# Optimization experiments

Hardware: AMD Instinct MI355X
Metric: run time of the kernel (lower is better)

Reference implementation:

```python
import jax, jax.numpy as jnp
import numpy as np

N = 5000
NFEAT = 512
NHID = 64
NHEADS = 8
NCLASS = 40
ALPHA = 0.2  # leaky relu slope
NEG_INF = -9e15


def setup_inputs() -> dict:
    key = jax.random.key(0)
    ks = jax.random.split(key, 12)
    x = jax.random.normal(ks[0], (N, NFEAT), dtype=jnp.float32)
    # binary adjacency, ~32 avg degree, with self loops
    adj = (jax.random.uniform(ks[1], (N, N)) < (32.0 / N)).astype(jnp.float32)
    adj = jnp.maximum(adj, jnp.eye(N, dtype=jnp.float32))
    s = 1.0 / np.sqrt(NFEAT)
    W_h = jax.random.uniform(ks[2], (NHEADS, NFEAT, NHID), minval=-s, maxval=s, dtype=jnp.float32)
    a_h = jax.random.uniform(ks[3], (NHEADS, 2 * NHID), minval=-s, maxval=s, dtype=jnp.float32)
    s2 = 1.0 / np.sqrt(NHID * NHEADS)
    W_o = jax.random.uniform(ks[4], (NHID * NHEADS, NHID), minval=-s2, maxval=s2, dtype=jnp.float32)
    a_o = jax.random.uniform(ks[5], (2 * NHID,), minval=-s2, maxval=s2, dtype=jnp.float32)
    s3 = 1.0 / np.sqrt(NHID)
    fc1_w = jax.random.uniform(ks[6], (NHID, 200), minval=-s3, maxval=s3, dtype=jnp.float32)
    fc1_b = jax.random.uniform(ks[7], (200,), minval=-s3, maxval=s3, dtype=jnp.float32)
    s4 = 1.0 / np.sqrt(200)
    fc2_w = jax.random.uniform(ks[8], (200, NCLASS), minval=-s4, maxval=s4, dtype=jnp.float32)
    fc2_b = jax.random.uniform(ks[9], (NCLASS,), minval=-s4, maxval=s4, dtype=jnp.float32)
    return {"x": x, "adj": adj, "W_h": W_h, "a_h": a_h, "W_o": W_o, "a_o": a_o,
            "fc1_w": fc1_w, "fc1_b": fc1_b, "fc2_w": fc2_w, "fc2_b": fc2_b}


def _masked_attention(e, adj):
    # e: [..., N, N]; mask where adj == 0, then row softmax
    e = jnp.where(adj > 0, e, NEG_INF)
    return jax.nn.softmax(e, axis=-1)


def reference(x, adj, W_h, a_h, W_o, a_o, fc1_w, fc1_b, fc2_w, fc2_b):
    # ---- multi-head GAT layer (concat=True), eval mode (dropout off) ----
    Wh = jnp.einsum('nf,hfo->hno', x, W_h)                 # [H, N, nhid]
    f1 = jnp.einsum('hno,ho->hn', Wh, a_h[:, :NHID])       # [H, N]
    f2 = jnp.einsum('hno,ho->hn', Wh, a_h[:, NHID:])       # [H, N]
    e = jax.nn.leaky_relu(f1[:, :, None] + f2[:, None, :], ALPHA)  # [H, N, N]
    att = _masked_attention(e, adj[None, :, :])
    h = jnp.einsum('hnm,hmo->hno', att, Wh)                # [H, N, nhid]
    h1 = jax.nn.elu(h).transpose(1, 0, 2).reshape(N, NHEADS * NHID)  # concat heads

    # ---- output GAT layer (concat=False) ----
    Wh2 = h1 @ W_o                                         # [N, nhid]
    g1 = Wh2 @ a_o[:NHID]                                  # [N]
    g2 = Wh2 @ a_o[NHID:]                                  # [N]
    e2 = jax.nn.leaky_relu(g1[:, None] + g2[None, :], ALPHA)
    att2 = _masked_attention(e2, adj)
    h2 = att2 @ Wh2                                        # [N, nhid]

    # ---- MLP head ----
    h3 = jax.nn.elu(h2 @ fc1_w + fc1_b)
    return h3 @ fc2_w + fc2_b                              # [N, nclass]
```

## Files before the change

kernel.cpp:

```cpp
#include <hip/hip_runtime.h>

typedef unsigned short u16;
typedef unsigned int u32;
typedef unsigned long long u64;
typedef __bf16 bf16_t;
typedef __bf16 bf16x8 __attribute__((ext_vector_type(8)));
typedef float f32x4 __attribute__((ext_vector_type(4)));
typedef u32 u32x4 __attribute__((ext_vector_type(4)));

#define NN 5000
#define NF 512
#define NH 64
#define HEADS 8
#define NCLS 40
#define CAP 128
#define LRELU 0.2f

#define CVT_BIG 320
#define CVT_GRID (CVT_BIG + 8)

__device__ __forceinline__ bool adj_is_bf16(const void* adj) {
    return ((*(const u32*)adj) & 0xFFFFu) != 0u;
}
__device__ __forceinline__ u16 rne_bf16(float f) {
    u32 u = __float_as_uint(f);
    u += 0x7FFFu + ((u >> 16) & 1u);
    return (u16)(u >> 16);
}
__device__ __forceinline__ float up_bf16(u16 h) {
    return __uint_as_float((u32)h << 16);
}
__device__ __forceinline__ u32x4 ntload4(const void* p, int idx) {
    return __builtin_nontemporal_load(((const u32x4*)p) + idx);
}

__global__ __launch_bounds__(256) void cvt(const void* __restrict__ x, const void* __restrict__ W_h,
                                           const void* __restrict__ adj,
                                           const void* a_h, const void* W_o, const void* a_o,
                                           const void* f1w, const void* f1b,
                                           const void* f2w, const void* f2b,
                                           u16* __restrict__ xc, u16* __restrict__ whc,
                                           float* a_hc, float* W_oc, float* a_oc,
                                           float* f1wc, float* f1bc, float* f2wc, float* f2bc) {
    const bool isb = adj_is_bf16(adj);
    const int b = blockIdx.x;
    if (b < CVT_BIG) {
        const int X4 = NN * NF / 4;
        const int T4 = X4 + HEADS * NF * NH / 4;
        for (int i = b * 256 + threadIdx.x; i < T4; i += CVT_BIG * 256) {
            const void* src; u16* dst; int off;
            if (i < X4) { src = x; dst = xc; off = i; }
            else        { src = W_h; dst = whc; off = i - X4; }
            ushort4 o;
            if (isb) {
                o = ((const ushort4*)src)[off];
            } else {
                u32x4 vv = ntload4(src, off);
                o.x = rne_bf16(__uint_as_float(vv[0])); o.y = rne_bf16(__uint_as_float(vv[1]));
                o.z = rne_bf16(__uint_as_float(vv[2])); o.w = rne_bf16(__uint_as_float(vv[3]));
            }
            ((ushort4*)dst)[off] = o;
        }
    } else {
        const int s0 = HEADS * 2 * NH, s1 = HEADS * NH * NH, s2 = 2 * NH,
                  s3 = NH * 200, s4 = 200, s5 = 200 * NCLS, s6 = NCLS;
        const int total = s0 + s1 + s2 + s3 + s4 + s5 + s6;
        for (int i = (b - CVT_BIG) * 256 + threadIdx.x; i < total; i += 8 * 256) {
            const void* src; float* dst; int off = i;
            if (off < s0) { src = a_h; dst = a_hc; }
            else if ((off -= s0) < s1) { src = W_o;  dst = W_oc; }
            else if ((off -= s1) < s2) { src = a_o;  dst = a_oc; }
            else if ((off -= s2) < s3) { src = f1w;  dst = f1wc; }
            else if ((off -= s3) < s4) { src = f1b;  dst = f1bc; }
            else if ((off -= s4) < s5) { src = f2w;  dst = f2wc; }
            else { off -= s5;           src = f2b;  dst = f2bc; }
            dst[off] = isb ? up_bf16(((const u16*)src)[off]) : ((const float*)src)[off];
        }
    }
}

__global__ __launch_bounds__(256) void gemm1_f(const bf16_t* __restrict__ x,
                                               const bf16_t* __restrict__ W_h,
                                               const float* __restrict__ a_h,
                                               float* __restrict__ Wh,
                                               float* __restrict__ f1,
                                               float* __restrict__ f2) {
    const int lane = threadIdx.x & 63;
    const int wid  = threadIdx.x >> 6;
    const int rg = blockIdx.x;
    const int h  = blockIdx.y;
    const int quad = lane >> 4;
    const int lr   = lane & 15;
    const int kq   = quad * 8;
    const int nCol = wid * 16 + lr;
    const bf16_t* Bh = W_h + (size_t)h * NF * NH;
    __shared__ float f1s[4][64], f2s[4][64];

    bf16x8 bfrag[16];
    #pragma unroll
    for (int s = 0; s < 16; ++s) {
        bf16x8 bb;
        #pragma unroll
        for (int j = 0; j < 8; ++j) bb[j] = Bh[(s * 32 + kq + j) * NH + nCol];
        bfrag[s] = bb;
    }
    const float a1c = a_h[h * 128 + nCol];
    const float a2c = a_h[h * 128 + NH + nCol];

    for (int t = 0; t < 4; ++t) {
        const int rb = rg * 64 + t * 16;
        int row  = rb + lr;
        int rowc = row < NN ? row : NN - 1;
        const bf16_t* xp = x + (size_t)rowc * NF + kq;
        f32x4 acc = {0.f, 0.f, 0.f, 0.f};
        #pragma unroll
        for (int s = 0; s < 16; ++s) {
            bf16x8 a = *(const bf16x8*)(xp + s * 32);
            acc = __builtin_amdgcn_mfma_f32_16x16x32_bf16(a, bfrag[s], acc, 0, 0, 0);
        }
        #pragma unroll
        for (int r = 0; r < 4; ++r) {
            int gr = rb + quad * 4 + r;
            if (gr < NN) Wh[(size_t)gr * (HEADS * NH) + h * NH + nCol] = acc[r];
            float p1 = acc[r] * a1c, p2 = acc[r] * a2c;
            #pragma unroll
            for (int o = 8; o; o >>= 1) { p1 += __shfl_xor(p1, o); p2 += __shfl_xor(p2, o); }
            if (lr == 0) { f1s[wid][t * 16 + quad * 4 + r] = p1; f2s[wid][t * 16 + quad * 4 + r] = p2; }
        }
    }
    __syncthreads();
    if (wid == 0) {
        int gr = rg * 64 + lane;
        if (gr < NN) {
            f1[h * NN + gr] = f1s[0][lane] + f1s[1][lane] + f1s[2][lane] + f1s[3][lane];
            f2[h * NN + gr] = f2s[0][lane] + f2s[1][lane] + f2s[2][lane] + f2s[3][lane];
        }
    }
}

__global__ __launch_bounds__(256) void agg1f(const void* __restrict__ adj,
                                             const float* __restrict__ Wh,
                                             const float* __restrict__ f1,
                                             const float* __restrict__ f2,
                                             int* __restrict__ nbr, int* __restrict__ deg,
                                             float* __restrict__ h1) {
    const bool isb = adj_is_bf16(adj);
    const int lane = threadIdx.x & 63;
    const int wid  = threadIdx.x >> 6;
    const int n = blockIdx.x;
    __shared__ int   s_seg[4][CAP];
    __shared__ int   s_cnt[4];
    __shared__ int   s_nbr[CAP];
    const u64 lt = (1ull << lane) - 1;

    int total = 0;
    if (!isb) {
        const float* row = (const float*)adj + (size_t)n * NN;
        const int c0 = wid * 313, cend = min(1250, c0 + 313);
        for (int base = c0; base < cend; base += 64) {
            int c = base + lane;
            u32x4 v = {0u, 0u, 0u, 0u};
            if (c < cend) v = ntload4(row, c);
            #pragma unroll
            for (int j = 0; j < 4; ++j) {
                bool nz = v[j] != 0u;
                u64 m = __ballot(nz);
                if (nz) { int pos = total + __popcll(m & lt); if (pos < CAP) s_seg[wid][pos] = c * 4 + j; }
                total += __popcll(m);
            }
        }
    } else {
        const u16* row = (const u16*)adj + (size_t)n * NN;
        const int c0 = wid * 157, cend = min(625, c0 + 157);
        for (int base = c0; base < cend; base += 64) {
            int c = base + lane;
            u32x4 v = {0u, 0u, 0u, 0u};
            if (c < cend) v = ntload4(row, c);
            #pragma unroll
            for (int j = 0; j < 4; ++j) {
                bool nz = (v[j] & 0xFFFFu) != 0u;
                u64 m = __ballot(nz);
                if (nz) { int pos = total + __popcll(m & lt); if (pos < CAP) s_seg[wid][pos] = c * 8 + 2 * j; }
                total += __popcll(m);
                bool nz2 = (v[j] >> 16) != 0u;
                u64 m2 = __ballot(nz2);
                if (nz2) { int pos = total + __popcll(m2 & lt); if (pos < CAP) s_seg[wid][pos] = c * 8 + 2 * j + 1; }
                total += __popcll(m2);
            }
        }
    }
    if (lane == 0) s_cnt[wid] = total < CAP ? total : CAP;
    __syncthreads();
    const int c0_ = s_cnt[0], c1_ = s_cnt[1], c2_ = s_cnt[2], c3_ = s_cnt[3];
    const int offw = (wid > 0 ? c0_ : 0) + (wid > 1 ? c1_ : 0) + (wid > 2 ? c2_ : 0);
    const int dall0 = c0_ + c1_ + c2_ + c3_;
    const int dall = dall0 < CAP ? dall0 : CAP;
    for (int i = lane; i < s_cnt[wid]; i += 64) {
        int p = offw + i;
        if (p < CAP) s_nbr[p] = s_seg[wid][i];
    }
    __syncthreads();
    for (int i = threadIdx.x; i < dall; i += 256) nbr[(size_t)n * CAP + i] = s_nbr[i];
    if (threadIdx.x == 0) deg[n] = dall;

    float s_alpha[CAP > 128 ? 4 : 2];
    #pragma unroll
    for (int rep = 0; rep < 2; ++rep) {
        const int h = wid + rep * 4;
        const float f1n = f1[h * NN + n];
        const float* f2h = f2 + (size_t)h * NN;
        float e0 = -INFINITY, e1 = -INFINITY;
        if (lane < dall) {
            float e = f1n + f2h[s_nbr[lane]];
            e0 = e > 0.f ? e : LRELU * e;
        }
        if (lane + 64 < dall) {
            float e = f1n + f2h[s_nbr[lane + 64]];
            e1 = e > 0.f ? e : LRELU * e;
        }
        float mx = fmaxf(e0, e1);
        #pragma unroll
        for (int o = 32; o; o >>= 1) mx = fmaxf(mx, __shfl_xor(mx, o));
        float p0 = lane < dall ? expf(e0 - mx) : 0.f;
        float p1 = lane + 64 < dall ? expf(e1 - mx) : 0.f;
        float sm = p0 + p1;
        #pragma unroll
        for (int o = 32; o; o >>= 1) sm += __shfl_xor(sm, o);

        __shared__ float s_al[4][CAP];
        s_al[wid][lane] = p0;
        s_al[wid][lane + 64] = p1;

        float acc0 = 0.f, acc1 = 0.f, acc2 = 0.f, acc3 = 0.f;
        const float* WhL = Wh + (size_t)h * NH + lane;
        int j = 0;
        for (; j + 4 <= dall; j += 4) {
            acc0 += s_al[wid][j]     * WhL[(size_t)s_nbr[j]     * (HEADS * NH)];
            acc1 += s_al[wid][j + 1] * WhL[(size_t)s_nbr[j + 1] * (HEADS * NH)];
            acc2 += s_al[wid][j + 2] * WhL[(size_t)s_nbr[j + 2] * (HEADS * NH)];
            acc3 += s_al[wid][j + 3] * WhL[(size_t)s_nbr[j + 3] * (HEADS * NH)];
        }
        for (; j < dall; ++j) acc0 += s_al[wid][j] * WhL[(size_t)s_nbr[j] * (HEADS * NH)];
        float hv = (acc0 + acc1 + acc2 + acc3) / sm;
        hv = hv > 0.f ? hv : expf(hv) - 1.f;
        h1[(size_t)n * (HEADS * NH) + h * NH + lane] = hv;
    }
}

__global__ __launch_bounds__(256) void gemm2_4(const float* __restrict__ h1,
                                               const float* __restrict__ W_o,
                                               const float* __restrict__ a_o,
                                               float* __restrict__ Wh2,
                                               float* __restrict__ g1,
                                               float* __restrict__ g2) {
    const int t = threadIdx.x;
    const int n0 = blockIdx.x * 4;
    __shared__ float sh[4 * 512];
    __shared__ float ps[4][4][64];
    const float4* src = (const float4*)(h1 + (size_t)n0 * 512);
    ((float4*)sh)[t]       = src[t];
    ((float4*)sh)[t + 256] = src[t + 256];
    __syncthreads();
    const int o = t & 63, part = t >> 6;
    float a0 = 0.f, a1 = 0.f, a2 = 0.f, a3 = 0.f;
    const float* wo = W_o + part * 128 * 64 + o;
    const float* s0 = sh + part * 128;
    #pragma unroll 4
    for (int f = 0; f < 128; ++f) {
        float w = wo[f * 64];
        a0 += s0[f] * w; a1 += s0[512 + f] * w; a2 += s0[1024 + f] * w; a3 += s0[1536 + f] * w;
    }
    ps[part][0][o] = a0; ps[part][1][o] = a1; ps[part][2][o] = a2; ps[part][3][o] = a3;
    __syncthreads();
    const int nd = t >> 6;
    float w2 = ps[0][nd][o] + ps[1][nd][o] + ps[2][nd][o] + ps[3][nd][o];
    Wh2[(size_t)(n0 + nd) * 64 + o] = w2;
    float p1 = w2 * a_o[o], p2 = w2 * a_o[64 + o];
    #pragma unroll
    for (int s = 32; s; s >>= 1) { p1 += __shfl_xor(p1, s); p2 += __shfl_xor(p2, s); }
    if (o == 0) { g1[n0 + nd] = p1; g2[n0 + nd] = p2; }
}

__global__ __launch_bounds__(256) void agg2_mlp(const float* __restrict__ Wh2,
                                                const float* __restrict__ g1,
                                                const float* __restrict__ g2,
                                                const int* __restrict__ nbr,
                                                const int* __restrict__ deg,
                                                const float* __restrict__ fc1_w,
                                                const float* __restrict__ fc1_b,
                                                const float* __restrict__ fc2_w,
                                                const float* __restrict__ fc2_b,
                                                float* __restrict__ out) {
    const int lane = threadIdx.x & 63;
    const int wid  = threadIdx.x >> 6;
    const int t = threadIdx.x;
    const int n0 = blockIdx.x * 4;
    const int n = n0 + wid;
    __shared__ float s_alpha[4][CAP];
    __shared__ int   s_nbr[4][CAP];
    __shared__ float s_h2[4][NH];
    __shared__ float s_h3[4][200];
    __shared__ float ps2[2][4][NCLS];
    const int d = deg[n];
    const int* nb = nbr + (size_t)n * CAP;
    const float gn = g1[n];

    float mx = -INFINITY;
    for (int j = lane; j < d; j += 64) {
        int m = nb[j];
        s_nbr[wid][j] = m;
        float e = gn + g2[m];
        e = e > 0.f ? e : LRELU * e;
        s_alpha[wid][j] = e;
        mx = fmaxf(mx, e);
    }
    #pragma unroll
    for (int o = 32; o; o >>= 1) mx = fmaxf(mx, __shfl_xor(mx, o));
    float sm = 0.f;
    for (int j = lane; j < d; j += 64) {
        float p = expf(s_alpha[wid][j] - mx);
        s_alpha[wid][j] = p;
        sm += p;
    }
    #pragma unroll
    for (int o = 32; o; o >>= 1) sm += __shfl_xor(sm, o);

    float acc0 = 0.f, acc1 = 0.f, acc2 = 0.f, acc3 = 0.f;
    int j = 0;
    for (; j + 4 <= d; j += 4) {
        acc0 += s_alpha[wid][j]     * Wh2[(size_t)s_nbr[wid][j]     * NH + lane];
        acc1 += s_alpha[wid][j + 1] * Wh2[(size_t)s_nbr[wid][j + 1] * NH + lane];
        acc2 += s_alpha[wid][j + 2] * Wh2[(size_t)s_nbr[wid][j + 2] * NH + lane];
        acc3 += s_alpha[wid][j + 3] * Wh2[(size_t)s_nbr[wid][j + 3] * NH + lane];
    }
    for (; j < d; ++j) acc0 += s_alpha[wid][j] * Wh2[(size_t)s_nbr[wid][j] * NH + lane];
    s_h2[wid][lane] = (acc0 + acc1 + acc2 + acc3) / sm;
    __syncthreads();

    if (t < 200) {
        float b0 = 0.f, b1 = 0.f, b2 = 0.f, b3 = 0.f;
        #pragma unroll 4
        for (int f = 0; f < NH; ++f) {
            float w = fc1_w[f * 200 + t];
            b0 += s_h2[0][f] * w; b1 += s_h2[1][f] * w; b2 += s_h2[2][f] * w; b3 += s_h2[3][f] * w;
        }
        float bb = fc1_b[t];
        b0 += bb; b1 += bb; b2 += bb; b3 += bb;
        s_h3[0][t] = b0 > 0.f ? b0 : expf(b0) - 1.f;
        s_h3[1][t] = b1 > 0.f ? b1 : expf(b1) - 1.f;
        s_h3[2][t] = b2 > 0.f ? b2 : expf(b2) - 1.f;
        s_h3[3][t] = b3 > 0.f ? b3 : expf(b3) - 1.f;
    }
    __syncthreads();

    if (t < 80) {
        const int o = t % 40, fh = t / 40;
        float c0 = 0.f, c1 = 0.f, c2 = 0.f, c3 = 0.f;
        #pragma unroll 4
        for (int f = fh * 100; f < fh * 100 + 100; ++f) {
            float w = fc2_w[f * NCLS + o];
            c0 += s_h3[0][f] * w; c1 += s_h3[1][f] * w; c2 += s_h3[2][f] * w; c3 += s_h3[3][f] * w;
        }
        ps2[fh][0][o] = c0; ps2[fh][1][o] = c1; ps2[fh][2][o] = c2; ps2[fh][3][o] = c3;
    }
    __syncthreads();
    if (t < 160) {
        const int nd = t / 40, o = t % 40;
        out[(size_t)(n0 + nd) * NCLS + o] = ps2[0][nd][o] + ps2[1][nd][o] + fc2_b[o];
    }
}

extern "C" void kernel_launch(void* const* d_in, const int* in_sizes, int n_in,
                              void* d_out, int out_size, void* d_ws, size_t ws_size,
                              hipStream_t stream) {
    const void* x     = d_in[0];
    const void* adj   = d_in[1];
    const void* W_h   = d_in[2];
    const void* a_h   = d_in[3];
    const void* W_o   = d_in[4];
    const void* a_o   = d_in[5];
    const void* fc1_w = d_in[6];
    const void* fc1_b = d_in[7];
    const void* fc2_w = d_in[8];
    const void* fc2_b = d_in[9];
    float* out = (float*)d_out;

    char* ws = (char*)d_ws;
    int*   nbr   = (int*)(ws + 0);
    int*   deg   = (int*)(ws + 2560000);
    float* Wh    = (float*)(ws + 2580000);
    float* f1    = (float*)(ws + 12820000);
    float* f2    = (float*)(ws + 12980000);
    float* h1    = (float*)(ws + 13140000);
    float* Wh2   = (float*)(ws + 23380000);
    float* g1    = (float*)(ws + 24660000);
    float* g2    = (float*)(ws + 24680000);
    u16*   xc    = (u16*)(ws + 24700000);
    u16*   whc   = (u16*)(ws + 29820000);
    float* a_hc  = (float*)(ws + 30344288);
    float* W_oc  = (float*)(ws + 30348384);
    float* a_oc  = (float*)(ws + 30479456);
    float* f1wc  = (float*)(ws + 30479968);
    float* f1bc  = (float*)(ws + 30531168);
    float* f2wc  = (float*)(ws + 30531968);
    float* f2bc  = (float*)(ws + 30563968);

    cvt<<<CVT_GRID, 256, 0, stream>>>(x, W_h, adj, a_h, W_o, a_o,
                                      fc1_w, fc1_b, fc2_w, fc2_b,
                                      xc, whc, a_hc, W_oc, a_oc,
                                      f1wc, f1bc, f2wc, f2bc);
    gemm1_f<<<dim3(79, HEADS), 256, 0, stream>>>((const bf16_t*)xc, (const bf16_t*)whc,
                                                 a_hc, Wh, f1, f2);
    agg1f<<<NN, 256, 0, stream>>>(adj, Wh, f1, f2, nbr, deg, h1);
    gemm2_4<<<NN / 4, 256, 0, stream>>>(h1, W_oc, a_oc, Wh2, g1, g2);
    agg2_mlp<<<NN / 4, 256, 0, stream>>>(Wh2, g1, g2, nbr, deg,
                                         f1wc, f1bc, f2wc, f2bc, out);
}
```

Measured before the change: 279.4 us.

## Batch adjacency row loads and fuse two heads' attention using shuffles

The adjacency scan now issues all of a wave's non-temporal row loads up front into a register array before the ballot/compaction pass, so the loads overlap instead of running one per iteration. The attention phase handles both heads of a wave together: neighbor indices and softmax weights stay in registers and are broadcast with shuffles instead of going through shared memory. Each neighbor row gather then serves both heads in one loop, which gives more memory-level parallelism. The cost is higher register pressure and many shuffle instructions per neighbor.

```diff
diff --git a/kernel.cpp b/kernel.cpp
--- a/kernel.cpp
+++ b/kernel.cpp
@@ -157,13 +157,18 @@
     if (!isb) {
         const float* row = (const float*)adj + (size_t)n * NN;
         const int c0 = wid * 313, cend = min(1250, c0 + 313);
-        for (int base = c0; base < cend; base += 64) {
-            int c = base + lane;
-            u32x4 v = {0u, 0u, 0u, 0u};
-            if (c < cend) v = ntload4(row, c);
+        u32x4 v[5];
+        #pragma unroll
+        for (int k = 0; k < 5; ++k) {
+            int c = c0 + k * 64 + lane;
+            v[k] = (c < cend) ? ntload4(row, c) : (u32x4){0u, 0u, 0u, 0u};
+        }
+        #pragma unroll
+        for (int k = 0; k < 5; ++k) {
+            int c = c0 + k * 64 + lane;
             #pragma unroll
             for (int j = 0; j < 4; ++j) {
-                bool nz = v[j] != 0u;
+                bool nz = v[k][j] != 0u;
                 u64 m = __ballot(nz);
                 if (nz) { int pos = total + __popcll(m & lt); if (pos < CAP) s_seg[wid][pos] = c * 4 + j; }
                 total += __popcll(m);
@@ -172,17 +177,22 @@
     } else {
         const u16* row = (const u16*)adj + (size_t)n * NN;
         const int c0 = wid * 157, cend = min(625, c0 + 157);
-        for (int base = c0; base < cend; base += 64) {
-            int c = base + lane;
-            u32x4 v = {0u, 0u, 0u, 0u};
-            if (c < cend) v = ntload4(row, c);
+        u32x4 v[3];
+        #pragma unroll
+        for (int k = 0; k < 3; ++k) {
+            int c = c0 + k * 64 + lane;
+            v[k] = (c < cend) ? ntload4(row, c) : (u32x4){0u, 0u, 0u, 0u};
+        }
+        #pragma unroll
+        for (int k = 0; k < 3; ++k) {
+            int c = c0 + k * 64 + lane;
             #pragma unroll
             for (int j = 0; j < 4; ++j) {
-                bool nz = (v[j] & 0xFFFFu) != 0u;
+                bool nz = (v[k][j] & 0xFFFFu) != 0u;
                 u64 m = __ballot(nz);
                 if (nz) { int pos = total + __popcll(m & lt); if (pos < CAP) s_seg[wid][pos] = c * 8 + 2 * j; }
                 total += __popcll(m);
-                bool nz2 = (v[j] >> 16) != 0u;
+                bool nz2 = (v[k][j] >> 16) != 0u;
                 u64 m2 = __ballot(nz2);
                 if (nz2) { int pos = total + __popcll(m2 & lt); if (pos < CAP) s_seg[wid][pos] = c * 8 + 2 * j + 1; }
                 total += __popcll(m2);
@@ -203,48 +213,73 @@
     for (int i = threadIdx.x; i < dall; i += 256) nbr[(size_t)n * CAP + i] = s_nbr[i];
     if (threadIdx.x == 0) deg[n] = dall;
 
-    float s_alpha[CAP > 128 ? 4 : 2];
-    #pragma unroll
-    for (int rep = 0; rep < 2; ++rep) {
-        const int h = wid + rep * 4;
-        const float f1n = f1[h * NN + n];
-        const float* f2h = f2 + (size_t)h * NN;
-        float e0 = -INFINITY, e1 = -INFINITY;
-        if (lane < dall) {
-            float e = f1n + f2h[s_nbr[lane]];
-            e0 = e > 0.f ? e : LRELU * e;
-        }
-        if (lane + 64 < dall) {
-            float e = f1n + f2h[s_nbr[lane + 64]];
-            e1 = e > 0.f ? e : LRELU * e;
-        }
-        float mx = fmaxf(e0, e1);
-        #pragma unroll
-        for (int o = 32; o; o >>= 1) mx = fmaxf(mx, __shfl_xor(mx, o));
-        float p0 = lane < dall ? expf(e0 - mx) : 0.f;
-        float p1 = lane + 64 < dall ? expf(e1 - mx) : 0.f;
-        float sm = p0 + p1;
-        #pragma unroll
-        for (int o = 32; o; o >>= 1) sm += __shfl_xor(sm, o);
-
-        __shared__ float s_al[4][CAP];
-        s_al[wid][lane] = p0;
-        s_al[wid][lane + 64] = p1;
-
-        float acc0 = 0.f, acc1 = 0.f, acc2 = 0.f, acc3 = 0.f;
-        const float* WhL = Wh + (size_t)h * NH + lane;
-        int j = 0;
-        for (; j + 4 <= dall; j += 4) {
-            acc0 += s_al[wid][j]     * WhL[(size_t)s_nbr[j]     * (HEADS * NH)];
-            acc1 += s_al[wid][j + 1] * WhL[(size_t)s_nbr[j + 1] * (HEADS * NH)];
-            acc2 += s_al[wid][j + 2] * WhL[(size_t)s_nbr[j + 2] * (HEADS * NH)];
-            acc3 += s_al[wid][j + 3] * WhL[(size_t)s_nbr[j + 3] * (HEADS * NH)];
-        }
-        for (; j < dall; ++j) acc0 += s_al[wid][j] * WhL[(size_t)s_nbr[j] * (HEADS * NH)];
-        float hv = (acc0 + acc1 + acc2 + acc3) / sm;
-        hv = hv > 0.f ? hv : expf(hv) - 1.f;
-        h1[(size_t)n * (HEADS * NH) + h * NH + lane] = hv;
-    }
+    const int ha = wid, hb = wid + 4;
+    const int nb0 = (lane < dall) ? s_nbr[lane] : 0;
+    const int nb1 = (lane + 64 < dall) ? s_nbr[lane + 64] : 0;
+    const float f10 = f1[ha * NN + n], f11 = f1[hb * NN + n];
+    const float* f2ha = f2 + (size_t)ha * NN;
+    const float* f2hb = f2 + (size_t)hb * NN;
+
+    float e00 = -INFINITY, e01 = -INFINITY, e10 = -INFINITY, e11 = -INFINITY;
+    if (lane < dall) {
+        float a = f10 + f2ha[nb0]; e00 = a > 0.f ? a : LRELU * a;
+        float b = f11 + f2hb[nb0]; e10 = b > 0.f ? b : LRELU * b;
+    }
+    if (lane + 64 < dall) {
+        float a = f10 + f2ha[nb1]; e01 = a > 0.f ? a : LRELU * a;
+        float b = f11 + f2hb[nb1]; e11 = b > 0.f ? b : LRELU * b;
+    }
+    float mx0 = fmaxf(e00, e01), mx1 = fmaxf(e10, e11);
+    #pragma unroll
+    for (int o = 32; o; o >>= 1) {
+        mx0 = fmaxf(mx0, __shfl_xor(mx0, o));
+        mx1 = fmaxf(mx1, __shfl_xor(mx1, o));
+    }
+    float p00 = lane < dall ? expf(e00 - mx0) : 0.f;
+    float p01 = lane + 64 < dall ? expf(e01 - mx0) : 0.f;
+    float p10 = lane < dall ? expf(e10 - mx1) : 0.f;
+    float p11 = lane + 64 < dall ? expf(e11 - mx1) : 0.f;
+    float sm0 = p00 + p01, sm1 = p10 + p11;
+    #pragma unroll
+    for (int o = 32; o; o >>= 1) { sm0 += __shfl_xor(sm0, o); sm1 += __shfl_xor(sm1, o); }
+
+    float A0 = 0.f, A1 = 0.f, A2 = 0.f, A3 = 0.f;
+    float B0 = 0.f, B1 = 0.f, B2 = 0.f, B3 = 0.f;
+    const float* W0 = Wh + ha * NH + lane;
+    const float* W1 = Wh + hb * NH + lane;
+    int j = 0;
+    for (; j + 4 <= dall; j += 4) {
+        #pragma unroll
+        for (int i = 0; i < 4; ++i) {
+            int jj = j + i;
+            int sl = jj & 63;
+            bool lo = jj < 64;
+            int   m  = lo ? __shfl(nb0, sl) : __shfl(nb1, sl);
+            float a0 = lo ? __shfl(p00, sl) : __shfl(p01, sl);
+            float a1 = lo ? __shfl(p10, sl) : __shfl(p11, sl);
+            size_t base = (size_t)m * (HEADS * NH);
+            float w0 = W0[base], w1 = W1[base];
+            if (i == 0) { A0 += a0 * w0; B0 += a1 * w1; }
+            else if (i == 1) { A1 += a0 * w0; B1 += a1 * w1; }
+            else if (i == 2) { A2 += a0 * w0; B2 += a1 * w1; }
+            else { A3 += a0 * w0; B3 += a1 * w1; }
+        }
+    }
+    for (; j < dall; ++j) {
+        int sl = j & 63;
+        bool lo = j < 64;
+        int   m  = lo ? __shfl(nb0, sl) : __shfl(nb1, sl);
+        float a0 = lo ? __shfl(p00, sl) : __shfl(p01, sl);
+        float a1 = lo ? __shfl(p10, sl) : __shfl(p11, sl);
+        size_t base = (size_t)m * (HEADS * NH);
+        A0 += a0 * W0[base]; B0 += a1 * W1[base];
+    }
+    float hv0 = (A0 + A1 + A2 + A3) / sm0;
+    float hv1 = (B0 + B1 + B2 + B3) / sm1;
+    hv0 = hv0 > 0.f ? hv0 : expf(hv0) - 1.f;
+    hv1 = hv1 > 0.f ? hv1 : expf(hv1) - 1.f;
+    h1[(size_t)n * (HEADS * NH) + ha * NH + lane] = hv0;
+    h1[(size_t)n * (HEADS * NH) + hb * NH + lane] = hv1;
 }
 
 __global__ __launch_bounds__(256) void gemm2_4(const float* __restrict__ h1,
```

Measured after the change: 278.3 us. About the same (-0.4%).
